# Kernel optimization log

Measured on AMD Instinct MI355X. Metric: run time of the kernel, lower is better.

The kernel has to match this reference:

```python
import jax, jax.numpy as jnp
import numpy as np

TEMP = 0.07


def setup_inputs() -> dict:
    key = jax.random.key(0)
    k1, k2 = jax.random.split(key)
    B, m, d = 256, 128, 768
    v_final = jax.random.normal(k1, (B, d), dtype=jnp.float32)
    T_fused = jax.random.normal(k2, (B, m, d), dtype=jnp.float32)
    return {"v_final": v_final, "T_fused": T_fused}


def reference(v_final, T_fused):
    B = v_final.shape[0]
    # [B, B, m] token-level similarities, scaled by temperature
    sim = jnp.einsum('id,jmd->ijm', v_final, T_fused) / TEMP
    # max over text tokens (ColBERT max-sim) -> [B, B]
    sim_max = sim.max(axis=-1)
    targets = jnp.arange(B)
    # symmetric cross-entropy with diagonal targets
    logp_i2t = jax.nn.log_softmax(sim_max, axis=-1)
    logp_t2i = jax.nn.log_softmax(sim_max.T, axis=-1)
    loss_i2t = -jnp.mean(logp_i2t[targets, targets])
    loss_t2i = -jnp.mean(logp_t2i[targets, targets])
    return (loss_i2t + loss_t2i) / 2
```

## Files before the change

### kernel.cpp

```cpp
#include <hip/hip_runtime.h>
#include <hip/hip_bf16.h>

constexpr int BATCH = 256;
constexpr int MTOK  = 128;
constexpr int DDIM  = 768;
constexpr int NV    = BATCH * DDIM;
constexpr float INV_TEMP = 1.0f / 0.07f;

typedef __bf16 bf16;
typedef __bf16 bf16x4 __attribute__((ext_vector_type(4)));
typedef __bf16 bf16x8 __attribute__((ext_vector_type(8)));
typedef float  f32x4  __attribute__((ext_vector_type(4)));

typedef __attribute__((address_space(3))) char       lds_char;
typedef const __attribute__((address_space(1))) char g_char;

__device__ __forceinline__ void async16(const void* g, void* l) {
    __builtin_amdgcn_global_load_lds((g_char*)g, (lds_char*)l, 16, 0, 0);
}

__global__ __launch_bounds__(256) void convert_v_kernel(
        const float4* __restrict__ v4, bf16x4* __restrict__ out) {
    int i = blockIdx.x * 256 + threadIdx.x;
    if (i >= NV / 4) return;
    float4 f = v4[i];
    bf16x4 o;
    o.x = (bf16)f.x; o.y = (bf16)f.y; o.z = (bf16)f.z; o.w = (bf16)f.w;
    out[i] = o;
}

__global__ __launch_bounds__(256, 2) void gemm_max_kernel(
        const bf16*  __restrict__ Vb,
        const float* __restrict__ T,
        float* __restrict__ Sp) {
    __shared__ char  lds[65536 + 8192];
    __shared__ float smax[256];

    const int jt   = blockIdx.x >> 1;
    const int mh   = blockIdx.x & 1;
    const int tid  = threadIdx.x;
    const int w    = tid >> 6;
    const int lane = tid & 63;
    const int quad = lane >> 4;
    const int l15  = lane & 15;

    const bf16* gA[8];
#pragma unroll
    for (int q = 0; q < 8; ++q) {
        int c = q * 256 + tid;
        int row = (c >> 2) & 255, sub = c & 3, kh = c >> 10;
        gA[q] = Vb + (size_t)row * DDIM + kh * 32 + sub * 8;
    }
    const int ldsAbase = (tid >> 6) * 1024;

    const float* gB[2];
    int boffw[2];
#pragma unroll
    for (int q = 0; q < 2; ++q) {
        int c = q * 256 + tid;
        int row = c >> 3, kp = c & 7;
        gB[q] = T + (size_t)(jt * MTOK + mh * 64 + row) * DDIM + kp * 8;
        boffw[q] = 65536 + (kp >> 2) * 4096 + row * 64 + (kp & 3) * 16;
    }

    int aoff[2][4], boff[2][4];
#pragma unroll
    for (int h = 0; h < 2; ++h)
#pragma unroll
        for (int t = 0; t < 4; ++t) {
            int ar = w * 64 + t * 16 + l15;
            aoff[h][t] = h * 16384 + ar * 64 + quad * 16;
            int br = t * 16 + l15;
            boff[h][t] = 65536 + h * 4096 + br * 64 + quad * 16;
        }

    f32x4 acc[4][4] = {};
    float4 pre[2][2];

#pragma unroll
    for (int q = 0; q < 8; ++q)
        async16(gA[q], lds + q * 4096 + ldsAbase);
#pragma unroll
    for (int q = 0; q < 2; ++q) {
        pre[q][0] = *(const float4*)(gB[q]);
        pre[q][1] = *(const float4*)(gB[q] + 4);
    }

    for (int kk = 0; kk < 12; ++kk) {
        const int buf = (kk & 1) * 32768;
#pragma unroll
        for (int q = 0; q < 2; ++q) {
            bf16x8 o;
            o[0] = (bf16)pre[q][0].x; o[1] = (bf16)pre[q][0].y;
            o[2] = (bf16)pre[q][0].z; o[3] = (bf16)pre[q][0].w;
            o[4] = (bf16)pre[q][1].x; o[5] = (bf16)pre[q][1].y;
            o[6] = (bf16)pre[q][1].z; o[7] = (bf16)pre[q][1].w;
            *(bf16x8*)(lds + boffw[q]) = o;
        }
        __syncthreads();

        if (kk < 11) {
            const int nbuf = ((kk + 1) & 1) * 32768;
#pragma unroll
            for (int q = 0; q < 8; ++q)
                async16(gA[q] + (kk + 1) * 64, lds + nbuf + q * 4096 + ldsAbase);
#pragma unroll
            for (int q = 0; q < 2; ++q) {
                const float* p = gB[q] + (kk + 1) * 64;
                pre[q][0] = *(const float4*)(p);
                pre[q][1] = *(const float4*)(p + 4);
            }
        }

#pragma unroll
        for (int h = 0; h < 2; ++h) {
            bf16x8 af[4], bb[4];
#pragma unroll
            for (int t = 0; t < 4; ++t) {
                af[t] = *(const bf16x8*)(lds + buf + aoff[h][t]);
                bb[t] = *(const bf16x8*)(lds + boff[h][t]);
            }
#pragma unroll
            for (int tr = 0; tr < 4; ++tr)
#pragma unroll
                for (int tc = 0; tc < 4; ++tc)
                    acc[tr][tc] = __builtin_amdgcn_mfma_f32_16x16x32_bf16(
                        af[tr], bb[tc], acc[tr][tc], 0, 0, 0);
        }
        __syncthreads();
    }

#pragma unroll
    for (int tr = 0; tr < 4; ++tr) {
#pragma unroll
        for (int r = 0; r < 4; ++r) {
            float v = acc[tr][0][r];
            v = fmaxf(v, acc[tr][1][r]);
            v = fmaxf(v, acc[tr][2][r]);
            v = fmaxf(v, acc[tr][3][r]);
            v = fmaxf(v, __shfl_xor(v, 1, 64));
            v = fmaxf(v, __shfl_xor(v, 2, 64));
            v = fmaxf(v, __shfl_xor(v, 4, 64));
            v = fmaxf(v, __shfl_xor(v, 8, 64));
            if (l15 == 0)
                smax[w * 64 + tr * 16 + quad * 4 + r] = v;
        }
    }
    __syncthreads();
    Sp[(size_t)mh * BATCH * BATCH + (size_t)jt * BATCH + tid] = smax[tid] * INV_TEMP;
}

__global__ __launch_bounds__(64) void ce1_kernel(
        const float* __restrict__ Sp, float* __restrict__ partial) {
    const int t = blockIdx.x;
    const int l = threadIdx.x;
    const float* Sp0 = Sp;
    const float* Sp1 = Sp + BATCH * BATCH;

    float vr[4], vc[4];
#pragma unroll
    for (int p = 0; p < 4; ++p) {
        int j = p * 64 + l;
        vr[p] = fmaxf(Sp0[j * BATCH + t], Sp1[j * BATCH + t]);
        int i = p * 64 + l;
        vc[p] = fmaxf(Sp0[t * BATCH + i], Sp1[t * BATCH + i]);
    }
    float mr = fmaxf(fmaxf(vr[0], vr[1]), fmaxf(vr[2], vr[3]));
    float mc = fmaxf(fmaxf(vc[0], vc[1]), fmaxf(vc[2], vc[3]));
    for (int o = 32; o > 0; o >>= 1) {
        mr = fmaxf(mr, __shfl_xor(mr, o, 64));
        mc = fmaxf(mc, __shfl_xor(mc, o, 64));
    }
    float sr = 0.f, sc = 0.f;
#pragma unroll
    for (int p = 0; p < 4; ++p) {
        sr += expf(vr[p] - mr);
        sc += expf(vc[p] - mc);
    }
    for (int o = 32; o > 0; o >>= 1) {
        sr += __shfl_xor(sr, o, 64);
        sc += __shfl_xor(sc, o, 64);
    }
    if (l == 0) {
        float diag = fmaxf(Sp0[t * BATCH + t], Sp1[t * BATCH + t]);
        partial[t] = 0.5f * ((mr + logf(sr)) + (mc + logf(sc))) - diag;
    }
}

__global__ __launch_bounds__(256) void ce2_kernel(
        const float* __restrict__ partial, float* __restrict__ out) {
    const int i = threadIdx.x;
    float term = partial[i];
    for (int o = 32; o > 0; o >>= 1) term += __shfl_down(term, o, 64);
    __shared__ float ps[4];
    if ((i & 63) == 0) ps[i >> 6] = term;
    __syncthreads();
    if (i == 0) out[0] = (ps[0] + ps[1] + ps[2] + ps[3]) / (float)BATCH;
}

extern "C" void kernel_launch(void* const* d_in, const int* in_sizes, int n_in,
                              void* d_out, int out_size, void* d_ws, size_t ws_size,
                              hipStream_t stream) {
    const float* v = (const float*)d_in[0];
    const float* T = (const float*)d_in[1];

    bf16*  Vb = (bf16*)d_ws;
    float* Sp = (float*)((char*)d_ws + (size_t)NV * sizeof(bf16));
    float* partial = Sp + 2 * BATCH * BATCH;

    convert_v_kernel<<<(NV / 4 + 255) / 256, 256, 0, stream>>>(
        (const float4*)v, (bf16x4*)Vb);
    gemm_max_kernel<<<512, 256, 0, stream>>>(Vb, T, Sp);
    ce1_kernel<<<256, 64, 0, stream>>>(Sp, partial);
    ce2_kernel<<<1, 256, 0, stream>>>(partial, (float*)d_out);
}
```

Before: 168.9 us.

## Drop LDS staging in GEMM-max and load MFMA fragments directly from global

The GEMM-max kernel no longer stages V and T tiles in shared memory through async global-to-LDS copies and barriers. Each wave now loads its own A and B fragments straight from global memory into registers and prefetches the next 32-wide k-step in registers. This removes LDS traffic and per-iteration __syncthreads. In exchange, every wave re-reads the same T rows (4x redundancy across the waves of a block), and the per-lane 16-byte loads are strided by rows, which relies on L1/L2 to absorb the reuse.

```diff
diff --git a/kernel.cpp b/kernel.cpp
--- a/kernel.cpp
+++ b/kernel.cpp
@@ -11,13 +11,6 @@
 typedef __bf16 bf16x4 __attribute__((ext_vector_type(4)));
 typedef __bf16 bf16x8 __attribute__((ext_vector_type(8)));
 typedef float  f32x4  __attribute__((ext_vector_type(4)));
-
-typedef __attribute__((address_space(3))) char       lds_char;
-typedef const __attribute__((address_space(1))) char g_char;
-
-__device__ __forceinline__ void async16(const void* g, void* l) {
-    __builtin_amdgcn_global_load_lds((g_char*)g, (lds_char*)l, 16, 0, 0);
-}
 
 __global__ __launch_bounds__(256) void convert_v_kernel(
         const float4* __restrict__ v4, bf16x4* __restrict__ out) {
@@ -33,101 +26,60 @@
         const bf16*  __restrict__ Vb,
         const float* __restrict__ T,
         float* __restrict__ Sp) {
-    __shared__ char  lds[65536 + 8192];
     __shared__ float smax[256];
 
     const int jt   = blockIdx.x >> 1;
-    const int mh   = blockIdx.x & 1;
+    const int nh   = blockIdx.x & 1;
     const int tid  = threadIdx.x;
     const int w    = tid >> 6;
     const int lane = tid & 63;
     const int quad = lane >> 4;
     const int l15  = lane & 15;
 
-    const bf16* gA[8];
+    const bf16* aptr[4];
+    const float* bptr[4];
 #pragma unroll
-    for (int q = 0; q < 8; ++q) {
-        int c = q * 256 + tid;
-        int row = (c >> 2) & 255, sub = c & 3, kh = c >> 10;
-        gA[q] = Vb + (size_t)row * DDIM + kh * 32 + sub * 8;
-    }
-    const int ldsAbase = (tid >> 6) * 1024;
-
-    const float* gB[2];
-    int boffw[2];
-#pragma unroll
-    for (int q = 0; q < 2; ++q) {
-        int c = q * 256 + tid;
-        int row = c >> 3, kp = c & 7;
-        gB[q] = T + (size_t)(jt * MTOK + mh * 64 + row) * DDIM + kp * 8;
-        boffw[q] = 65536 + (kp >> 2) * 4096 + row * 64 + (kp & 3) * 16;
+    for (int t = 0; t < 4; ++t) {
+        aptr[t] = Vb + (size_t)(w * 64 + t * 16 + l15) * DDIM + quad * 8;
+        bptr[t] = T + (size_t)(jt * MTOK + nh * 64 + t * 16 + l15) * DDIM + quad * 8;
     }
 
-    int aoff[2][4], boff[2][4];
+    f32x4 acc[4][4] = {};
+
+    bf16x8 apre[4];
+    float4 bpre[4][2];
 #pragma unroll
-    for (int h = 0; h < 2; ++h)
+    for (int t = 0; t < 4; ++t) {
+        apre[t]    = *(const bf16x8*)(aptr[t]);
+        bpre[t][0] = *(const float4*)(bptr[t]);
+        bpre[t][1] = *(const float4*)(bptr[t] + 4);
+    }
+
+    for (int s = 0; s < 24; ++s) {
+        bf16x8 af[4], bb[4];
 #pragma unroll
         for (int t = 0; t < 4; ++t) {
-            int ar = w * 64 + t * 16 + l15;
-            aoff[h][t] = h * 16384 + ar * 64 + quad * 16;
-            int br = t * 16 + l15;
-            boff[h][t] = 65536 + h * 4096 + br * 64 + quad * 16;
+            af[t] = apre[t];
+            bb[t][0] = (bf16)bpre[t][0].x; bb[t][1] = (bf16)bpre[t][0].y;
+            bb[t][2] = (bf16)bpre[t][0].z; bb[t][3] = (bf16)bpre[t][0].w;
+            bb[t][4] = (bf16)bpre[t][1].x; bb[t][5] = (bf16)bpre[t][1].y;
+            bb[t][6] = (bf16)bpre[t][1].z; bb[t][7] = (bf16)bpre[t][1].w;
         }
-
-    f32x4 acc[4][4] = {};
-    float4 pre[2][2];
-
+        if (s < 23) {
+            const int ko = (s + 1) * 32;
 #pragma unroll
-    for (int q = 0; q < 8; ++q)
-        async16(gA[q], lds + q * 4096 + ldsAbase);
-#pragma unroll
-    for (int q = 0; q < 2; ++q) {
-        pre[q][0] = *(const float4*)(gB[q]);
-        pre[q][1] = *(const float4*)(gB[q] + 4);
-    }
-
-    for (int kk = 0; kk < 12; ++kk) {
-        const int buf = (kk & 1) * 32768;
-#pragma unroll
-        for (int q = 0; q < 2; ++q) {
-            bf16x8 o;
-            o[0] = (bf16)pre[q][0].x; o[1] = (bf16)pre[q][0].y;
-            o[2] = (bf16)pre[q][0].z; o[3] = (bf16)pre[q][0].w;
-            o[4] = (bf16)pre[q][1].x; o[5] = (bf16)pre[q][1].y;
-            o[6] = (bf16)pre[q][1].z; o[7] = (bf16)pre[q][1].w;
-            *(bf16x8*)(lds + boffw[q]) = o;
-        }
-        __syncthreads();
-
-        if (kk < 11) {
-            const int nbuf = ((kk + 1) & 1) * 32768;
-#pragma unroll
-            for (int q = 0; q < 8; ++q)
-                async16(gA[q] + (kk + 1) * 64, lds + nbuf + q * 4096 + ldsAbase);
-#pragma unroll
-            for (int q = 0; q < 2; ++q) {
-                const float* p = gB[q] + (kk + 1) * 64;
-                pre[q][0] = *(const float4*)(p);
-                pre[q][1] = *(const float4*)(p + 4);
+            for (int t = 0; t < 4; ++t) {
+                apre[t]    = *(const bf16x8*)(aptr[t] + ko);
+                bpre[t][0] = *(const float4*)(bptr[t] + ko);
+                bpre[t][1] = *(const float4*)(bptr[t] + ko + 4);
             }
         }
-
 #pragma unroll
-        for (int h = 0; h < 2; ++h) {
-            bf16x8 af[4], bb[4];
+        for (int tr = 0; tr < 4; ++tr)
 #pragma unroll
-            for (int t = 0; t < 4; ++t) {
-                af[t] = *(const bf16x8*)(lds + buf + aoff[h][t]);
-                bb[t] = *(const bf16x8*)(lds + boff[h][t]);
-            }
-#pragma unroll
-            for (int tr = 0; tr < 4; ++tr)
-#pragma unroll
-                for (int tc = 0; tc < 4; ++tc)
-                    acc[tr][tc] = __builtin_amdgcn_mfma_f32_16x16x32_bf16(
-                        af[tr], bb[tc], acc[tr][tc], 0, 0, 0);
-        }
-        __syncthreads();
+            for (int tc = 0; tc < 4; ++tc)
+                acc[tr][tc] = __builtin_amdgcn_mfma_f32_16x16x32_bf16(
+                    af[tr], bb[tc], acc[tr][tc], 0, 0, 0);
     }
 
 #pragma unroll
@@ -147,7 +99,7 @@
         }
     }
     __syncthreads();
-    Sp[(size_t)mh * BATCH * BATCH + (size_t)jt * BATCH + tid] = smax[tid] * INV_TEMP;
+    Sp[(size_t)nh * BATCH * BATCH + (size_t)jt * BATCH + tid] = smax[tid] * INV_TEMP;
 }
 
 __global__ __launch_bounds__(64) void ce1_kernel(
```

New measurement: 198.3 us. +17.4%, slower.
